# Kernel optimization log

Hardware: AMD Instinct MI355X
Metric: run time of the kernel (lower is better)

The kernel has to match this reference:

```python
import jax, jax.numpy as jnp
import numpy as np

T, N, C, D, K = 512, 256, 128, 128, 128

def setup_inputs() -> dict:
    key = jax.random.key(0)
    ks = jax.random.split(key, 6)
    s = 1.0 / np.sqrt(D)
    return {
        "x":   jax.random.normal(ks[0], (T, N, C), dtype=jnp.float32),
        "W_x": jax.random.normal(ks[1], (D, C), dtype=jnp.float32) * s,  # torch Linear: (out,in)
        "b_x": jax.random.normal(ks[2], (D,), dtype=jnp.float32) * s,
        "W_h": jax.random.normal(ks[3], (D, D), dtype=jnp.float32) * s,
        "W_y": jax.random.normal(ks[4], (K, D), dtype=jnp.float32) * s,
        "b_y": jax.random.normal(ks[5], (K,), dtype=jnp.float32) * s,
    }

def reference(x, W_x, b_x, W_h, W_y, b_y):
    # Elman RNN: h_t = relu(x_t @ W_x^T + b_x + h_{t-1} @ W_h^T)
    # Precompute the input projection for all timesteps in one big GEMM,
    # then scan only the true recurrent dependency.
    xproj = jnp.einsum('tnc,dc->tnd', x, W_x) + b_x  # (T, N, D)

    def step(h, xp_t):
        h_new = jax.nn.relu(xp_t + h @ W_h.T)  # (N, D)
        return h_new, h_new

    h0 = jnp.zeros((x.shape[1], W_h.shape[0]), dtype=x.dtype)
    _, all_h = jax.lax.scan(step, h0, xproj)          # (T, N, D)
    all_y = jnp.einsum('tnd,kd->tnk', all_h, W_y) + b_y  # (T, N, K)
    return all_y, all_h
```

## Files before the change

kernel.cpp:

```cpp
#include <hip/hip_runtime.h>

static constexpr int T_STEPS = 512;
static constexpr int NBATCH  = 256;
static constexpr int DD      = 128;
static constexpr long TND    = (long)T_STEPS * NBATCH * DD;

typedef short bf16x8 __attribute__((ext_vector_type(8)));
typedef float f32x4  __attribute__((ext_vector_type(4)));
typedef unsigned u32x4 __attribute__((ext_vector_type(4)));

__device__ inline unsigned short f2bf(float f) {
  unsigned u = __builtin_bit_cast(unsigned, f);
  unsigned r = u + 0x7FFFu + ((u >> 16) & 1u);
  return (unsigned short)(r >> 16);
}

__device__ inline bf16x8 pack8(const float* s) {
  bf16x8 v;
#pragma unroll
  for (int i = 0; i < 8; ++i) v[i] = (short)f2bf(s[i]);
  return v;
}

__device__ __forceinline__ unsigned cvtpk_bf16(float lo, float hi) {
  unsigned r;
  asm("v_cvt_pk_bf16_f32 %0, %1, %2" : "=v"(r) : "v"(lo), "v"(hi));
  return r;
}

__global__ __launch_bounds__(256) void cvt_x_bf16(
    const float* __restrict__ x, unsigned short* __restrict__ xb, long n8) {
  long i = (long)blockIdx.x * 256 + threadIdx.x;
  const long stride = (long)gridDim.x * 256;
  for (; i < n8; i += stride) {
    const float* p = x + i * 8;
    f32x4 a = *(const f32x4*)p, b = *(const f32x4*)(p + 4);
    u32x4 u;
    u[0] = cvtpk_bf16(a[0], a[1]); u[1] = cvtpk_bf16(a[2], a[3]);
    u[2] = cvtpk_bf16(b[0], b[1]); u[3] = cvtpk_bf16(b[2], b[3]);
    *(u32x4*)(xb + i * 8) = u;
  }
}

__global__ __launch_bounds__(256) void gemm128_yT(
    const float* __restrict__ A, const float* __restrict__ W,
    const float* __restrict__ bias, float* __restrict__ O, int ntiles) {
  const int lane = threadIdx.x & 63;
  const int wib  = threadIdx.x >> 6;
  const int m    = lane & 15;
  const int q    = lane >> 4;

  bf16x8 Wf[8][4];
#pragma unroll
  for (int j = 0; j < 8; ++j)
#pragma unroll
    for (int kq = 0; kq < 4; ++kq) {
      const float* p = W + (j * 16 + m) * DD + kq * 32 + q * 8;
      float t[8];
      *(float4*)&t[0] = *(const float4*)p;
      *(float4*)&t[4] = *(const float4*)(p + 4);
      Wf[j][kq] = pack8(t);
    }
  f32x4 bv4[8];
#pragma unroll
  for (int j = 0; j < 8; ++j) bv4[j] = *(const f32x4*)(bias + j * 16 + 4 * q);

  const int wglobal = blockIdx.x * 4 + wib;
  const int nwaves  = gridDim.x * 4;
#pragma unroll 2
  for (int tile = wglobal; tile < ntiles; tile += nwaves) {
    const long r0 = (long)tile * 16;

    bf16x8 af[4];
#pragma unroll
    for (int kq = 0; kq < 4; ++kq) {
      const float* p = A + (r0 + m) * DD + kq * 32 + q * 8;
      f32x4 lo = *(const f32x4*)p, hi = *(const f32x4*)(p + 4);
      u32x4 u;
      u[0] = cvtpk_bf16(lo[0], lo[1]); u[1] = cvtpk_bf16(lo[2], lo[3]);
      u[2] = cvtpk_bf16(hi[0], hi[1]); u[3] = cvtpk_bf16(hi[2], hi[3]);
      af[kq] = __builtin_bit_cast(bf16x8, u);
    }
    f32x4 acc[8];
#pragma unroll
    for (int j = 0; j < 8; ++j)
      acc[j] = __builtin_amdgcn_mfma_f32_16x16x32_bf16(Wf[j][0], af[0], bv4[j], 0, 0, 0);
#pragma unroll
    for (int kq = 1; kq < 4; ++kq)
#pragma unroll
      for (int j = 0; j < 8; ++j)
        acc[j] = __builtin_amdgcn_mfma_f32_16x16x32_bf16(Wf[j][kq], af[kq], acc[j], 0, 0, 0);

    float* op = O + (r0 + m) * DD + 4 * q;
#pragma unroll
    for (int j = 0; j < 8; ++j)
      *(f32x4*)(op + j * 16) = acc[j];
  }
}

__global__ __launch_bounds__(256, 1) void rnn_scan_fused(
    const unsigned short* __restrict__ xbf, const float* __restrict__ Wx,
    const float* __restrict__ bx, const float* __restrict__ Wh,
    float* __restrict__ H ) {
  __shared__ __align__(16) u32x4 xchg[2][4][64];

  const int wv   = threadIdx.x >> 6;
  const int lane = threadIdx.x & 63;
  const int m = lane & 15;
  const int q = lane >> 4;

  xchg[1][wv][lane] = (u32x4){0u, 0u, 0u, 0u};
  __syncthreads();

  const int jj0 = 2 * wv;

  bf16x8 Wxf[2][4];
#pragma unroll
  for (int jl = 0; jl < 2; ++jl)
#pragma unroll
    for (int kq = 0; kq < 4; ++kq) {
      const float* p = Wx + ((jj0 + jl) * 16 + m) * DD + kq * 32 + q * 8;
      float t[8];
      *(float4*)&t[0] = *(const float4*)p;
      *(float4*)&t[4] = *(const float4*)(p + 4);
      Wxf[jl][kq] = pack8(t);
    }
  bf16x8 Whf[2][4];
#pragma unroll
  for (int jl = 0; jl < 2; ++jl)
#pragma unroll
    for (int kq = 0; kq < 4; ++kq) {
      const float* p = Wh + ((jj0 + jl) * 16 + m) * DD + kq * 32 + 4 * q;
      float t[8];
      *(float4*)&t[0] = *(const float4*)p;
      *(float4*)&t[4] = *(const float4*)(p + 16);
      Whf[jl][kq] = pack8(t);
    }
  f32x4 bxv[2];
#pragma unroll
  for (int jl = 0; jl < 2; ++jl)
    bxv[jl] = *(const f32x4*)(bx + (jj0 + jl) * 16 + 4 * q);

  const long stepN = (long)NBATCH * DD;
  const unsigned short* xb = xbf + (long)(blockIdx.x * 16 + m) * DD + 8 * q;
  float* hb = H + (long)(blockIdx.x * 16 + m) * DD;

  auto pref = [&](bf16x8 (&r)[4], int t) {
    const unsigned short* p = xb + (long)t * stepN;
#pragma unroll
    for (int kq = 0; kq < 4; ++kq) r[kq] = *(const bf16x8*)(p + 32 * kq);
  };

  const f32x4 zz = (f32x4){0.f, 0.f, 0.f, 0.f};

  f32x4 xw0a, xw0b, xw1a, xw1b;

  auto xw_compute = [&](const bf16x8 (&xf)[4]) {
    xw0a = __builtin_amdgcn_mfma_f32_16x16x32_bf16(Wxf[0][0], xf[0], bxv[0], 0, 0, 0);
    xw1a = __builtin_amdgcn_mfma_f32_16x16x32_bf16(Wxf[1][0], xf[0], bxv[1], 0, 0, 0);
    xw0b = __builtin_amdgcn_mfma_f32_16x16x32_bf16(Wxf[0][2], xf[2], zz, 0, 0, 0);
    xw1b = __builtin_amdgcn_mfma_f32_16x16x32_bf16(Wxf[1][2], xf[2], zz, 0, 0, 0);
    xw0a = __builtin_amdgcn_mfma_f32_16x16x32_bf16(Wxf[0][1], xf[1], xw0a, 0, 0, 0);
    xw1a = __builtin_amdgcn_mfma_f32_16x16x32_bf16(Wxf[1][1], xf[1], xw1a, 0, 0, 0);
    xw0b = __builtin_amdgcn_mfma_f32_16x16x32_bf16(Wxf[0][3], xf[3], xw0b, 0, 0, 0);
    xw1b = __builtin_amdgcn_mfma_f32_16x16x32_bf16(Wxf[1][3], xf[3], xw1b, 0, 0, 0);
  };

  auto step = [&](const bf16x8 (&xfn)[4], int t, int par) {
    bf16x8 b0 = __builtin_bit_cast(bf16x8, xchg[par ^ 1][0][lane]);
    bf16x8 b1 = __builtin_bit_cast(bf16x8, xchg[par ^ 1][1][lane]);
    bf16x8 b2 = __builtin_bit_cast(bf16x8, xchg[par ^ 1][2][lane]);
    bf16x8 b3 = __builtin_bit_cast(bf16x8, xchg[par ^ 1][3][lane]);

    f32x4 h0a = __builtin_amdgcn_mfma_f32_16x16x32_bf16(Whf[0][0], b0, zz, 0, 0, 0);
    f32x4 h1a = __builtin_amdgcn_mfma_f32_16x16x32_bf16(Whf[1][0], b0, zz, 0, 0, 0);
    f32x4 h0b = __builtin_amdgcn_mfma_f32_16x16x32_bf16(Whf[0][2], b2, zz, 0, 0, 0);
    f32x4 h1b = __builtin_amdgcn_mfma_f32_16x16x32_bf16(Whf[1][2], b2, zz, 0, 0, 0);
    h0a = __builtin_amdgcn_mfma_f32_16x16x32_bf16(Whf[0][1], b1, h0a, 0, 0, 0);
    h1a = __builtin_amdgcn_mfma_f32_16x16x32_bf16(Whf[1][1], b1, h1a, 0, 0, 0);
    h0b = __builtin_amdgcn_mfma_f32_16x16x32_bf16(Whf[0][3], b3, h0b, 0, 0, 0);
    h1b = __builtin_amdgcn_mfma_f32_16x16x32_bf16(Whf[1][3], b3, h1b, 0, 0, 0);

    f32x4 s0 = (xw0a + xw0b) + (h0a + h0b);
    f32x4 s1 = (xw1a + xw1b) + (h1a + h1b);
    f32x4 h0, h1;
#pragma unroll
    for (int r = 0; r < 4; ++r) { h0[r] = fmaxf(s0[r], 0.f); h1[r] = fmaxf(s1[r], 0.f); }

    u32x4 own;
    own[0] = cvtpk_bf16(h0[0], h0[1]); own[1] = cvtpk_bf16(h0[2], h0[3]);
    own[2] = cvtpk_bf16(h1[0], h1[1]); own[3] = cvtpk_bf16(h1[2], h1[3]);
    xchg[par][wv][lane] = own;

    asm volatile("s_waitcnt lgkmcnt(0)" ::: "memory");
    __builtin_amdgcn_s_barrier();
    __builtin_amdgcn_sched_barrier(0);

    float* hp = hb + (long)t * stepN;
    *(f32x4*)(hp + (jj0 + 0) * 16 + 4 * q) = h0;
    *(f32x4*)(hp + (jj0 + 1) * 16 + 4 * q) = h1;
    xw_compute(xfn);
  };

  bf16x8 sA[4], sB[4], sC[4], sD[4];
  pref(sA, 0);
  pref(sB, 1); pref(sC, 2); pref(sD, 3);
  xw_compute(sA);
  pref(sA, 4);

#pragma unroll 1
  for (int t = 0; t < T_STEPS; t += 4) {
    step(sB, t, 0);     pref(sB, t + 5 < T_STEPS ? t + 5 : T_STEPS - 1);
    step(sC, t + 1, 1); pref(sC, t + 6 < T_STEPS ? t + 6 : T_STEPS - 1);
    step(sD, t + 2, 0); pref(sD, t + 7 < T_STEPS ? t + 7 : T_STEPS - 1);
    step(sA, t + 3, 1); pref(sA, t + 8 < T_STEPS ? t + 8 : T_STEPS - 1);
  }
}

extern "C" void kernel_launch(void* const* d_in, const int* in_sizes, int n_in,
                              void* d_out, int out_size, void* d_ws, size_t ws_size,
                              hipStream_t stream) {
  const float* x  = (const float*)d_in[0];
  const float* Wx = (const float*)d_in[1];
  const float* bx = (const float*)d_in[2];
  const float* Wh = (const float*)d_in[3];
  const float* Wy = (const float*)d_in[4];
  const float* by = (const float*)d_in[5];

  float* Y = (float*)d_out;
  float* H = (float*)d_out + TND;

  unsigned short* xbf = (unsigned short*)Y;

  const int ntiles = T_STEPS * NBATCH / 16;

  cvt_x_bf16<<<2048, 256, 0, stream>>>(x, xbf, TND / 8);
  rnn_scan_fused<<<NBATCH / 16, 256, 0, stream>>>(xbf, Wx, bx, Wh, H);
  gemm128_yT<<<512, 256, 0, stream>>>(H, Wy, by, Y, ntiles);
}
```

Baseline: 474.9 us.

## Fuse output projection into recurrent scan using exchanged bf16 hidden state

```diff
diff --git a/kernel.cpp b/kernel.cpp
--- a/kernel.cpp
+++ b/kernel.cpp
@@ -98,10 +98,12 @@
   }
 }
 
+template <bool FUSE_Y>
 __global__ __launch_bounds__(256, 1) void rnn_scan_fused(
     const unsigned short* __restrict__ xbf, const float* __restrict__ Wx,
     const float* __restrict__ bx, const float* __restrict__ Wh,
-    float* __restrict__ H ) {
+    const float* __restrict__ Wy, const float* __restrict__ by,
+    float* __restrict__ H, float* __restrict__ Y) {
   __shared__ __align__(16) u32x4 xchg[2][4][64];
 
   const int wv   = threadIdx.x >> 6;
@@ -125,7 +127,7 @@
       *(float4*)&t[4] = *(const float4*)(p + 4);
       Wxf[jl][kq] = pack8(t);
     }
-  bf16x8 Whf[2][4];
+  bf16x8 Whf[2][4], Wyf[2][4];
 #pragma unroll
   for (int jl = 0; jl < 2; ++jl)
 #pragma unroll
@@ -135,15 +137,24 @@
       *(float4*)&t[0] = *(const float4*)p;
       *(float4*)&t[4] = *(const float4*)(p + 16);
       Whf[jl][kq] = pack8(t);
-    }
-  f32x4 bxv[2];
-#pragma unroll
-  for (int jl = 0; jl < 2; ++jl)
+      if constexpr (FUSE_Y) {
+        const float* py = Wy + ((jj0 + jl) * 16 + m) * DD + kq * 32 + 4 * q;
+        *(float4*)&t[0] = *(const float4*)py;
+        *(float4*)&t[4] = *(const float4*)(py + 16);
+        Wyf[jl][kq] = pack8(t);
+      }
+    }
+  f32x4 bxv[2], byv[2];
+#pragma unroll
+  for (int jl = 0; jl < 2; ++jl) {
     bxv[jl] = *(const f32x4*)(bx + (jj0 + jl) * 16 + 4 * q);
+    if constexpr (FUSE_Y) byv[jl] = *(const f32x4*)(by + (jj0 + jl) * 16 + 4 * q);
+  }
 
   const long stepN = (long)NBATCH * DD;
   const unsigned short* xb = xbf + (long)(blockIdx.x * 16 + m) * DD + 8 * q;
   float* hb = H + (long)(blockIdx.x * 16 + m) * DD;
+  float* yb = Y + (long)(blockIdx.x * 16 + m) * DD;
 
   auto pref = [&](bf16x8 (&r)[4], int t) {
     const unsigned short* p = xb + (long)t * stepN;
@@ -166,6 +177,20 @@
     xw1b = __builtin_amdgcn_mfma_f32_16x16x32_bf16(Wxf[1][3], xf[3], xw1b, 0, 0, 0);
   };
 
+  auto y_compute_store = [&](bf16x8 c0, bf16x8 c1, bf16x8 c2, bf16x8 c3, int ty) {
+    f32x4 y0 = __builtin_amdgcn_mfma_f32_16x16x32_bf16(Wyf[0][0], c0, byv[0], 0, 0, 0);
+    f32x4 y1 = __builtin_amdgcn_mfma_f32_16x16x32_bf16(Wyf[1][0], c0, byv[1], 0, 0, 0);
+    y0 = __builtin_amdgcn_mfma_f32_16x16x32_bf16(Wyf[0][1], c1, y0, 0, 0, 0);
+    y1 = __builtin_amdgcn_mfma_f32_16x16x32_bf16(Wyf[1][1], c1, y1, 0, 0, 0);
+    y0 = __builtin_amdgcn_mfma_f32_16x16x32_bf16(Wyf[0][2], c2, y0, 0, 0, 0);
+    y1 = __builtin_amdgcn_mfma_f32_16x16x32_bf16(Wyf[1][2], c2, y1, 0, 0, 0);
+    y0 = __builtin_amdgcn_mfma_f32_16x16x32_bf16(Wyf[0][3], c3, y0, 0, 0, 0);
+    y1 = __builtin_amdgcn_mfma_f32_16x16x32_bf16(Wyf[1][3], c3, y1, 0, 0, 0);
+    float* yp = yb + (long)ty * stepN;
+    *(f32x4*)(yp + (jj0 + 0) * 16 + 4 * q) = y0;
+    *(f32x4*)(yp + (jj0 + 1) * 16 + 4 * q) = y1;
+  };
+
   auto step = [&](const bf16x8 (&xfn)[4], int t, int par) {
     bf16x8 b0 = __builtin_bit_cast(bf16x8, xchg[par ^ 1][0][lane]);
     bf16x8 b1 = __builtin_bit_cast(bf16x8, xchg[par ^ 1][1][lane]);
@@ -199,6 +224,9 @@
     float* hp = hb + (long)t * stepN;
     *(f32x4*)(hp + (jj0 + 0) * 16 + 4 * q) = h0;
     *(f32x4*)(hp + (jj0 + 1) * 16 + 4 * q) = h1;
+    if constexpr (FUSE_Y) {
+      if (t) y_compute_store(b0, b1, b2, b3, t - 1);
+    }
     xw_compute(xfn);
   };
 
@@ -214,6 +242,14 @@
     step(sC, t + 1, 1); pref(sC, t + 6 < T_STEPS ? t + 6 : T_STEPS - 1);
     step(sD, t + 2, 0); pref(sD, t + 7 < T_STEPS ? t + 7 : T_STEPS - 1);
     step(sA, t + 3, 1); pref(sA, t + 8 < T_STEPS ? t + 8 : T_STEPS - 1);
+  }
+
+  if constexpr (FUSE_Y) {
+    bf16x8 c0 = __builtin_bit_cast(bf16x8, xchg[1][0][lane]);
+    bf16x8 c1 = __builtin_bit_cast(bf16x8, xchg[1][1][lane]);
+    bf16x8 c2 = __builtin_bit_cast(bf16x8, xchg[1][2][lane]);
+    bf16x8 c3 = __builtin_bit_cast(bf16x8, xchg[1][3][lane]);
+    y_compute_store(c0, c1, c2, c3, T_STEPS - 1);
   }
 }
 
@@ -230,11 +266,19 @@
   float* Y = (float*)d_out;
   float* H = (float*)d_out + TND;
 
-  unsigned short* xbf = (unsigned short*)Y;
-
-  const int ntiles = T_STEPS * NBATCH / 16;
-
-  cvt_x_bf16<<<2048, 256, 0, stream>>>(x, xbf, TND / 8);
-  rnn_scan_fused<<<NBATCH / 16, 256, 0, stream>>>(xbf, Wx, bx, Wh, H);
-  gemm128_yT<<<512, 256, 0, stream>>>(H, Wy, by, Y, ntiles);
-}
+  const size_t xbf_bytes = (size_t)TND * sizeof(unsigned short);
+
+  if (d_ws != nullptr && ws_size >= xbf_bytes) {
+    unsigned short* xbf = (unsigned short*)d_ws;
+    cvt_x_bf16<<<2048, 256, 0, stream>>>(x, xbf, TND / 8);
+    rnn_scan_fused<true><<<NBATCH / 16, 256, 0, stream>>>(
+        xbf, Wx, bx, Wh, Wy, by, H, Y);
+  } else {
+    unsigned short* xbf = (unsigned short*)Y;
+    const int ntiles = T_STEPS * NBATCH / 16;
+    cvt_x_bf16<<<2048, 256, 0, stream>>>(x, xbf, TND / 8);
+    rnn_scan_fused<false><<<NBATCH / 16, 256, 0, stream>>>(
+        xbf, Wx, bx, Wh, Wy, by, H, Y);
+    gemm128_yT<<<512, 256, 0, stream>>>(H, Wy, by, Y, ntiles);
+  }
+}
```

Result: slower. 569.0 us (+19.8%).
